# Kernel tuning notes

Measured on AMD Instinct MI355X. Metric: run time of the kernel, lower is better.

The kernel has to match this reference:

```python
import jax, jax.numpy as jnp
import numpy as np

N, D, S, C = 2048, 1024, 49, 1000


def setup_inputs() -> dict:
    key = jax.random.key(0)
    k1, k2, k3 = jax.random.split(key, 3)
    x = jax.random.normal(k1, (N, D, S), dtype=jnp.float32)
    mu = jax.random.normal(k2, (C, D), dtype=jnp.float32)
    # precision = inverse covariance -> symmetric PSD; build a well-conditioned one
    R = jax.random.normal(k3, (D, D), dtype=jnp.float32)
    precision = (R @ R.T) / D + jnp.eye(D, dtype=jnp.float32)
    return {"x": x, "mu": mu, "precision": precision}


def reference(x, mu, precision):
    # z: [N, D] global-average-pooled features (z.view(N, D, -1).mean(2))
    z = jnp.mean(x, axis=2)
    # score[n, c] = -0.5 * (z_n - mu_c) @ P @ (z_n - mu_c)
    # Expanded to avoid materializing [N, C, D]:
    #   zPz - z P mu - mu P z + mu P mu   (no symmetry assumption on P)
    zP = z @ precision                      # [N, D]
    zPt = z @ precision.T                   # [N, D]
    qz = jnp.sum(zP * z, axis=1)            # [N]   diag(z P z^T)
    cross1 = zP @ mu.T                      # [N, C] z P mu
    cross2 = zPt @ mu.T                     # [N, C] mu P z
    qmu = jnp.einsum('cd,de,ce->c', mu, precision, mu)  # [C]
    score = -0.5 * (qz[:, None] - cross1 - cross2 + qmu[None, :])
    return score
```

## Files before the change

### kernel.cpp

```cpp
#include <hip/hip_runtime.h>
#include <hip/hip_bf16.h>

typedef unsigned short u16;
typedef __bf16 bf16x8 __attribute__((ext_vector_type(8)));
typedef float f32x4 __attribute__((ext_vector_type(4)));

typedef const __attribute__((address_space(1))) void gv_t;
typedef __attribute__((address_space(3))) void lv_t;

#define NN 2048
#define DD 1024
#define SS 49
#define CC 1000
#define CP 1024

#define BK 64
#define KK DD

__device__ inline u16 f2bf(float f) {
    __hip_bfloat16 h = __float2bfloat16(f);
    union { __hip_bfloat16 h; u16 u; } cv; cv.h = h; return cv.u;
}

__device__ __forceinline__ void gemm64_core(const u16* __restrict__ A,
                                            const u16* __restrict__ Bt,
                                            int m0, int n0, char* smem,
                                            f32x4 acc[2][2], int tid) {
    char* As = smem;
    char* Bs = smem + 16384;
    const int lane = tid & 63;
    const int wr = (tid >> 6) >> 1, wc = (tid >> 6) & 1;
    const int r16 = lane & 15, hk = lane >> 4;
    const char* Ab = (const char*)A;
    const char* Bb = (const char*)Bt;

    auto stage = [&](int buf, int k0) {
        #pragma unroll
        for (int j = 0; j < 2; j++) {
            const int c = j * 256 + tid;
            const int row = c >> 3, slot = c & 7;
            const int goff = ((slot ^ (row & 7)) << 4);
            __builtin_amdgcn_global_load_lds(
                (gv_t*)(Ab + ((size_t)(m0 + row) * KK + k0) * 2 + goff),
                (lv_t*)(As + buf * 8192 + c * 16), 16, 0, 0);
            __builtin_amdgcn_global_load_lds(
                (gv_t*)(Bb + ((size_t)(n0 + row) * KK + k0) * 2 + goff),
                (lv_t*)(Bs + buf * 8192 + c * 16), 16, 0, 0);
        }
    };

    const int nt = KK / BK;
    stage(0, 0);
    __syncthreads();
    int cur = 0;
    for (int kt = 0; kt < nt; ++kt) {
        if (kt + 1 < nt) stage(cur ^ 1, (kt + 1) * BK);
        bf16x8 a[2][2], b[2][2];
        #pragma unroll
        for (int mi = 0; mi < 2; mi++) {
            const int row = wr * 32 + mi * 16 + r16;
            #pragma unroll
            for (int kk2 = 0; kk2 < 2; kk2++) {
                const int g = kk2 * 4 + hk;
                a[mi][kk2] = *(const bf16x8*)(As + cur * 8192 + row * 128 + ((g ^ (row & 7)) << 4));
            }
        }
        #pragma unroll
        for (int ni = 0; ni < 2; ni++) {
            const int row = wc * 32 + ni * 16 + r16;
            #pragma unroll
            for (int kk2 = 0; kk2 < 2; kk2++) {
                const int g = kk2 * 4 + hk;
                b[ni][kk2] = *(const bf16x8*)(Bs + cur * 8192 + row * 128 + ((g ^ (row & 7)) << 4));
            }
        }
        #pragma unroll
        for (int kk2 = 0; kk2 < 2; kk2++)
            #pragma unroll
            for (int mi = 0; mi < 2; mi++)
                #pragma unroll
                for (int ni = 0; ni < 2; ni++)
                    acc[mi][ni] = __builtin_amdgcn_mfma_f32_16x16x32_bf16(
                        a[mi][kk2], b[ni][kk2], acc[mi][ni], 0, 0, 0);
        __syncthreads();
        cur ^= 1;
    }
}

__global__ __launch_bounds__(256) void prep_k(const float* __restrict__ P,
                                              const float* __restrict__ mu,
                                              u16* __restrict__ q,
                                              u16* __restrict__ mu_bf,
                                              float* __restrict__ qzh,
                                              float* __restrict__ qmuh) {
    int i = blockIdx.x * 256 + threadIdx.x;
    int r = i >> 10, c = i & 1023;
    q[i]     = f2bf(P[i] + P[c * DD + r]);
    mu_bf[i] = f2bf(r < CC ? mu[i] : 0.f);
    if (i < NN) qzh[i]  = 0.f;
    if (i < CP) qmuh[i] = 0.f;
}

__global__ __launch_bounds__(256) void pool_muq_k(const float* __restrict__ x,
                                                  const u16* __restrict__ q,
                                                  const u16* __restrict__ mu_bf,
                                                  const float* __restrict__ mu,
                                                  u16* __restrict__ b_bf,
                                                  float* __restrict__ qmuh,
                                                  float* __restrict__ zf,
                                                  u16* __restrict__ zb) {
    __shared__ char smem[50176];
    const int tid = threadIdx.x;
    const int bid = blockIdx.x;

    if (bid >= 256) {
        const int u = bid - 256;
        float* lds = (float*)smem;
        const size_t base = (size_t)u * (256 * SS);
        const float4* src = (const float4*)(x + base);
        float4* dst = (float4*)lds;
        #pragma unroll
        for (int i = 0; i < 13; i++) {
            int idx = i * 256 + tid;
            if (idx < (256 * SS) / 4) dst[idx] = src[idx];
        }
        __syncthreads();
        const float* r = lds + tid * SS;
        float s = 0.f;
        #pragma unroll
        for (int j = 0; j < SS; j++) s += r[j];
        s *= (1.f / 49.f);
        size_t o = (size_t)u * 256 + tid;
        zf[o] = s;
        zb[o] = f2bf(s);
        return;
    }

    const int m0 = (bid >> 4) * 64, n0 = (bid & 15) * 64;
    f32x4 acc[2][2] = {};
    gemm64_core(mu_bf, q, m0, n0, smem, acc, tid);

    const int lane = tid & 63;
    const int wr = (tid >> 6) >> 1, wc = (tid >> 6) & 1;
    const int cr = (lane >> 4) * 4, cc2 = lane & 15;
    #pragma unroll
    for (int mi = 0; mi < 2; mi++) {
        const int gr0 = m0 + wr * 32 + mi * 16 + cr;
        #pragma unroll
        for (int r = 0; r < 4; r++) {
            const int row = gr0 + r;
            float v = 0.f;
            #pragma unroll
            for (int ni = 0; ni < 2; ni++) {
                const int gc = n0 + wc * 32 + ni * 16 + cc2;
                float av = acc[mi][ni][r];
                float sv = (row < CC) ? mu[(size_t)row * DD + gc] : 0.f;
                v += av * sv;
                b_bf[(size_t)row * DD + gc] = f2bf(av);
            }
            #pragma unroll
            for (int m = 1; m < 16; m <<= 1) v += __shfl_xor(v, m);
            if (cc2 == 0) atomicAdd(qmuh + row, 0.25f * v);
        }
    }
}

__global__ __launch_bounds__(256) void zgemm_k(const u16* __restrict__ z_bf,
                                               const u16* __restrict__ q,
                                               const u16* __restrict__ b_bf,
                                               const float* __restrict__ zf,
                                               const float* __restrict__ qmuh,
                                               float* __restrict__ qzh,
                                               float* __restrict__ part) {
    __shared__ char smem[32768];
    const int tid = threadIdx.x;
    const int bid = blockIdx.x;
    const bool isScore = (bid < 512);
    const int i = isScore ? bid : bid - 512;
    const int m0 = (i >> 4) * 64, n0 = (i & 15) * 64;

    f32x4 acc[2][2] = {};
    gemm64_core(z_bf, isScore ? b_bf : q, m0, n0, smem, acc, tid);

    const int lane = tid & 63;
    const int wr = (tid >> 6) >> 1, wc = (tid >> 6) & 1;
    const int cr = (lane >> 4) * 4, cc2 = lane & 15;
    if (isScore) {
        #pragma unroll
        for (int mi = 0; mi < 2; mi++) {
            #pragma unroll
            for (int ni = 0; ni < 2; ni++) {
                const int gr = m0 + wr * 32 + mi * 16 + cr;
                const int gc = n0 + wc * 32 + ni * 16 + cc2;
                const float qm = qmuh[gc];
                #pragma unroll
                for (int r = 0; r < 4; r++)
                    part[(size_t)(gr + r) * CP + gc] = 0.5f * acc[mi][ni][r] - qm;
            }
        }
    } else {
        #pragma unroll
        for (int mi = 0; mi < 2; mi++) {
            const int gr0 = m0 + wr * 32 + mi * 16 + cr;
            #pragma unroll
            for (int r = 0; r < 4; r++) {
                const int row = gr0 + r;
                float v = 0.f;
                #pragma unroll
                for (int ni = 0; ni < 2; ni++) {
                    const int gc = n0 + wc * 32 + ni * 16 + cc2;
                    v += acc[mi][ni][r] * zf[(size_t)row * DD + gc];
                }
                #pragma unroll
                for (int m = 1; m < 16; m <<= 1) v += __shfl_xor(v, m);
                if (cc2 == 0) atomicAdd(qzh + row, 0.25f * v);
            }
        }
    }
}

__global__ __launch_bounds__(256) void finish_k(const float* __restrict__ part,
                                                const float* __restrict__ qzh,
                                                float* __restrict__ out) {
    const int n = blockIdx.x, tid = threadIdx.x;
    if (tid >= 250) return;
    const float qz = qzh[n];
    float4 p = *(const float4*)(part + (size_t)n * CP + tid * 4);
    float4 o = { p.x - qz, p.y - qz, p.z - qz, p.w - qz };
    *(float4*)(out + (size_t)n * CC + tid * 4) = o;
}

extern "C" void kernel_launch(void* const* d_in, const int* in_sizes, int n_in,
                              void* d_out, int out_size, void* d_ws, size_t ws_size,
                              hipStream_t stream) {
    const float* x  = (const float*)d_in[0];
    const float* mu = (const float*)d_in[1];
    const float* P  = (const float*)d_in[2];
    float* out = (float*)d_out;

    char* w = (char*)d_ws;
    u16*   q_bf  = (u16*)w;   w += (size_t)DD * DD * 2;
    u16*   mu_bf = (u16*)w;   w += (size_t)CP * DD * 2;
    u16*   b_bf  = (u16*)w;   w += (size_t)CP * DD * 2;
    u16*   z_bf  = (u16*)w;   w += (size_t)NN * DD * 2;
    float* zf    = (float*)w; w += (size_t)NN * DD * 4;
    float* part  = (float*)w; w += (size_t)NN * CP * 4;
    float* qzh   = (float*)w; w += (size_t)NN * 4;
    float* qmuh  = (float*)w;

    prep_k<<<(DD * DD) / 256, 256, 0, stream>>>(P, mu, q_bf, mu_bf, qzh, qmuh);
    pool_muq_k<<<256 + (NN * DD) / 256, 256, 0, stream>>>(
        x, q_bf, mu_bf, mu, b_bf, qmuh, zf, z_bf);
    zgemm_k<<<1024, 256, 0, stream>>>(z_bf, q_bf, b_bf, zf, qmuh, qzh, part);
    finish_k<<<NN, 256, 0, stream>>>(part, qzh, out);
}
```

Baseline: 119.3 us.

## Restage kernels to overlap pooling with GEMMs and triple-buffer the GEMM core

Pooling of x is split across two launches. The first half runs alongside the precision/mu conversion, and the second half runs alongside the mu·Q GEMM and the first half of the z·Q GEMM. The score GEMM is split by row halves so that it writes the final output directly, with qz and qmu subtracted in its epilogue. This removes the partial buffer and the finish kernel. The GEMM inner loop moves from double to triple buffering, with explicit vmcnt waits and a single barrier per k-step, which raises shared memory use to 48KB per block.

```diff
diff --git a/kernel.cpp b/kernel.cpp
--- a/kernel.cpp
+++ b/kernel.cpp
@@ -16,6 +16,7 @@
 
 #define BK 64
 #define KK DD
+#define NT (KK / BK)
 
 __device__ inline u16 f2bf(float f) {
     __hip_bfloat16 h = __float2bfloat16(f);
@@ -26,8 +27,6 @@
                                             const u16* __restrict__ Bt,
                                             int m0, int n0, char* smem,
                                             f32x4 acc[2][2], int tid) {
-    char* As = smem;
-    char* Bs = smem + 16384;
     const int lane = tid & 63;
     const int wr = (tid >> 6) >> 1, wc = (tid >> 6) & 1;
     const int r16 = lane & 15, hk = lane >> 4;
@@ -42,19 +41,24 @@
             const int goff = ((slot ^ (row & 7)) << 4);
             __builtin_amdgcn_global_load_lds(
                 (gv_t*)(Ab + ((size_t)(m0 + row) * KK + k0) * 2 + goff),
-                (lv_t*)(As + buf * 8192 + c * 16), 16, 0, 0);
+                (lv_t*)(smem + buf * 16384 + c * 16), 16, 0, 0);
             __builtin_amdgcn_global_load_lds(
                 (gv_t*)(Bb + ((size_t)(n0 + row) * KK + k0) * 2 + goff),
-                (lv_t*)(Bs + buf * 8192 + c * 16), 16, 0, 0);
+                (lv_t*)(smem + buf * 16384 + 8192 + c * 16), 16, 0, 0);
         }
     };
 
-    const int nt = KK / BK;
     stage(0, 0);
-    __syncthreads();
-    int cur = 0;
-    for (int kt = 0; kt < nt; ++kt) {
-        if (kt + 1 < nt) stage(cur ^ 1, (kt + 1) * BK);
+    stage(1, BK);
+    for (int t = 0; t < NT; ++t) {
+        if (t + 1 < NT) asm volatile("s_waitcnt vmcnt(4)" ::: "memory");
+        else            asm volatile("s_waitcnt vmcnt(0)" ::: "memory");
+        __builtin_amdgcn_s_barrier();
+        __builtin_amdgcn_sched_barrier(0);
+        if (t + 2 < NT) stage((t + 2) % 3, (t + 2) * BK);
+
+        const char* As = smem + (t % 3) * 16384;
+        const char* Bs = As + 8192;
         bf16x8 a[2][2], b[2][2];
         #pragma unroll
         for (int mi = 0; mi < 2; mi++) {
@@ -62,7 +66,7 @@
             #pragma unroll
             for (int kk2 = 0; kk2 < 2; kk2++) {
                 const int g = kk2 * 4 + hk;
-                a[mi][kk2] = *(const bf16x8*)(As + cur * 8192 + row * 128 + ((g ^ (row & 7)) << 4));
+                a[mi][kk2] = *(const bf16x8*)(As + row * 128 + ((g ^ (row & 7)) << 4));
             }
         }
         #pragma unroll
@@ -71,7 +75,7 @@
             #pragma unroll
             for (int kk2 = 0; kk2 < 2; kk2++) {
                 const int g = kk2 * 4 + hk;
-                b[ni][kk2] = *(const bf16x8*)(Bs + cur * 8192 + row * 128 + ((g ^ (row & 7)) << 4));
+                b[ni][kk2] = *(const bf16x8*)(Bs + row * 128 + ((g ^ (row & 7)) << 4));
             }
         }
         #pragma unroll
@@ -82,64 +86,37 @@
                 for (int ni = 0; ni < 2; ni++)
                     acc[mi][ni] = __builtin_amdgcn_mfma_f32_16x16x32_bf16(
                         a[mi][kk2], b[ni][kk2], acc[mi][ni], 0, 0, 0);
-        __syncthreads();
-        cur ^= 1;
-    }
-}
-
-__global__ __launch_bounds__(256) void prep_k(const float* __restrict__ P,
-                                              const float* __restrict__ mu,
-                                              u16* __restrict__ q,
-                                              u16* __restrict__ mu_bf,
-                                              float* __restrict__ qzh,
-                                              float* __restrict__ qmuh) {
-    int i = blockIdx.x * 256 + threadIdx.x;
-    int r = i >> 10, c = i & 1023;
-    q[i]     = f2bf(P[i] + P[c * DD + r]);
-    mu_bf[i] = f2bf(r < CC ? mu[i] : 0.f);
-    if (i < NN) qzh[i]  = 0.f;
-    if (i < CP) qmuh[i] = 0.f;
-}
-
-__global__ __launch_bounds__(256) void pool_muq_k(const float* __restrict__ x,
-                                                  const u16* __restrict__ q,
-                                                  const u16* __restrict__ mu_bf,
-                                                  const float* __restrict__ mu,
-                                                  u16* __restrict__ b_bf,
-                                                  float* __restrict__ qmuh,
-                                                  float* __restrict__ zf,
-                                                  u16* __restrict__ zb) {
-    __shared__ char smem[50176];
-    const int tid = threadIdx.x;
-    const int bid = blockIdx.x;
-
-    if (bid >= 256) {
-        const int u = bid - 256;
-        float* lds = (float*)smem;
-        const size_t base = (size_t)u * (256 * SS);
-        const float4* src = (const float4*)(x + base);
-        float4* dst = (float4*)lds;
-        #pragma unroll
-        for (int i = 0; i < 13; i++) {
-            int idx = i * 256 + tid;
-            if (idx < (256 * SS) / 4) dst[idx] = src[idx];
-        }
-        __syncthreads();
-        const float* r = lds + tid * SS;
-        float s = 0.f;
-        #pragma unroll
-        for (int j = 0; j < SS; j++) s += r[j];
-        s *= (1.f / 49.f);
-        size_t o = (size_t)u * 256 + tid;
-        zf[o] = s;
-        zb[o] = f2bf(s);
-        return;
-    }
-
-    const int m0 = (bid >> 4) * 64, n0 = (bid & 15) * 64;
-    f32x4 acc[2][2] = {};
-    gemm64_core(mu_bf, q, m0, n0, smem, acc, tid);
-
+    }
+}
+
+
+__device__ __forceinline__ void pool_unit(const float* __restrict__ x, int u,
+                                          float* __restrict__ zf,
+                                          u16* __restrict__ zb,
+                                          char* smem, int tid) {
+    float* lds = (float*)smem;
+    const size_t base = (size_t)u * (256 * SS);
+    const float4* src = (const float4*)(x + base);
+    float4* dst = (float4*)lds;
+    #pragma unroll
+    for (int i = 0; i < 13; i++) {
+        int idx = i * 256 + tid;
+        if (idx < (256 * SS) / 4) dst[idx] = src[idx];
+    }
+    __syncthreads();
+    const float* r = lds + tid * SS;
+    float s = 0.f;
+    #pragma unroll
+    for (int j = 0; j < SS; j++) s += r[j];
+    s *= (1.f / 49.f);
+    size_t o = (size_t)u * 256 + tid;
+    zf[o] = s;
+    zb[o] = f2bf(s);
+}
+
+__device__ __forceinline__ void zqd_epi(const f32x4 acc[2][2], int m0, int n0,
+                                        const float* __restrict__ zf,
+                                        float* __restrict__ qzh, int tid) {
     const int lane = tid & 63;
     const int wr = (tid >> 6) >> 1, wc = (tid >> 6) & 1;
     const int cr = (lane >> 4) * 4, cc2 = lane & 15;
@@ -153,52 +130,82 @@
             #pragma unroll
             for (int ni = 0; ni < 2; ni++) {
                 const int gc = n0 + wc * 32 + ni * 16 + cc2;
-                float av = acc[mi][ni][r];
-                float sv = (row < CC) ? mu[(size_t)row * DD + gc] : 0.f;
-                v += av * sv;
-                b_bf[(size_t)row * DD + gc] = f2bf(av);
+                v += acc[mi][ni][r] * zf[(size_t)row * DD + gc];
             }
             #pragma unroll
             for (int m = 1; m < 16; m <<= 1) v += __shfl_xor(v, m);
-            if (cc2 == 0) atomicAdd(qmuh + row, 0.25f * v);
-        }
-    }
-}
-
-__global__ __launch_bounds__(256) void zgemm_k(const u16* __restrict__ z_bf,
-                                               const u16* __restrict__ q,
-                                               const u16* __restrict__ b_bf,
-                                               const float* __restrict__ zf,
-                                               const float* __restrict__ qmuh,
-                                               float* __restrict__ qzh,
-                                               float* __restrict__ part) {
-    __shared__ char smem[32768];
-    const int tid = threadIdx.x;
-    const int bid = blockIdx.x;
-    const bool isScore = (bid < 512);
-    const int i = isScore ? bid : bid - 512;
-    const int m0 = (i >> 4) * 64, n0 = (i & 15) * 64;
-
-    f32x4 acc[2][2] = {};
-    gemm64_core(z_bf, isScore ? b_bf : q, m0, n0, smem, acc, tid);
-
+            if (cc2 == 0) atomicAdd(qzh + row, 0.25f * v);
+        }
+    }
+}
+
+__device__ __forceinline__ void score_epi(const f32x4 acc[2][2], int m0, int n0,
+                                          const float* __restrict__ qzh,
+                                          const float* __restrict__ qmuh,
+                                          float* __restrict__ out, int tid) {
     const int lane = tid & 63;
     const int wr = (tid >> 6) >> 1, wc = (tid >> 6) & 1;
     const int cr = (lane >> 4) * 4, cc2 = lane & 15;
-    if (isScore) {
-        #pragma unroll
-        for (int mi = 0; mi < 2; mi++) {
-            #pragma unroll
-            for (int ni = 0; ni < 2; ni++) {
-                const int gr = m0 + wr * 32 + mi * 16 + cr;
-                const int gc = n0 + wc * 32 + ni * 16 + cc2;
+    #pragma unroll
+    for (int mi = 0; mi < 2; mi++) {
+        #pragma unroll
+        for (int ni = 0; ni < 2; ni++) {
+            const int gr = m0 + wr * 32 + mi * 16 + cr;
+            const int gc = n0 + wc * 32 + ni * 16 + cc2;
+            if (gc < CC) {
                 const float qm = qmuh[gc];
                 #pragma unroll
                 for (int r = 0; r < 4; r++)
-                    part[(size_t)(gr + r) * CP + gc] = 0.5f * acc[mi][ni][r] - qm;
-            }
-        }
+                    out[(size_t)(gr + r) * CC + gc] =
+                        0.5f * acc[mi][ni][r] - qzh[gr + r] - qm;
+            }
+        }
+    }
+}
+
+__global__ __launch_bounds__(256) void l1a_k(const float* __restrict__ x,
+                                             const float* __restrict__ P,
+                                             const float* __restrict__ mu,
+                                             u16* __restrict__ q,
+                                             u16* __restrict__ mu_bf,
+                                             float* __restrict__ zf,
+                                             u16* __restrict__ zb,
+                                             float* __restrict__ qzh,
+                                             float* __restrict__ qmuh) {
+    __shared__ char smem[50176];
+    const int tid = threadIdx.x, bid = blockIdx.x;
+    if (bid < 4096) {
+        int i = bid * 256 + tid;
+        int r = i >> 10, c = i & 1023;
+        q[i]     = f2bf(P[i] + P[c * DD + r]);
+        mu_bf[i] = f2bf(r < CC ? mu[i] : 0.f);
+        if (i < NN) qzh[i]  = 0.f;
+        if (i < CP) qmuh[i] = 0.f;
     } else {
+        pool_unit(x, bid - 4096, zf, zb, smem, tid);
+    }
+}
+
+__global__ __launch_bounds__(256) void l1b_k(const float* __restrict__ x,
+                                             const u16* __restrict__ q,
+                                             const u16* __restrict__ mu_bf,
+                                             const float* __restrict__ mu,
+                                             const u16* __restrict__ z_bf,
+                                             u16* __restrict__ b_bf,
+                                             float* __restrict__ qmuh,
+                                             const float* __restrict__ zf,
+                                             float* __restrict__ zf_w,
+                                             u16* __restrict__ zb_w,
+                                             float* __restrict__ qzh) {
+    __shared__ char smem[50176];
+    const int tid = threadIdx.x, bid = blockIdx.x;
+    if (bid < 256) {
+        const int m0 = (bid >> 4) * 64, n0 = (bid & 15) * 64;
+        f32x4 acc[2][2] = {};
+        gemm64_core(mu_bf, q, m0, n0, smem, acc, tid);
+        const int lane = tid & 63;
+        const int wr = (tid >> 6) >> 1, wc = (tid >> 6) & 1;
+        const int cr = (lane >> 4) * 4, cc2 = lane & 15;
         #pragma unroll
         for (int mi = 0; mi < 2; mi++) {
             const int gr0 = m0 + wr * 32 + mi * 16 + cr;
@@ -209,25 +216,61 @@
                 #pragma unroll
                 for (int ni = 0; ni < 2; ni++) {
                     const int gc = n0 + wc * 32 + ni * 16 + cc2;
-                    v += acc[mi][ni][r] * zf[(size_t)row * DD + gc];
+                    float av = acc[mi][ni][r];
+                    float sv = (row < CC) ? mu[(size_t)row * DD + gc] : 0.f;
+                    v += av * sv;
+                    b_bf[(size_t)row * DD + gc] = f2bf(av);
                 }
                 #pragma unroll
                 for (int m = 1; m < 16; m <<= 1) v += __shfl_xor(v, m);
-                if (cc2 == 0) atomicAdd(qzh + row, 0.25f * v);
-            }
-        }
-    }
-}
-
-__global__ __launch_bounds__(256) void finish_k(const float* __restrict__ part,
-                                                const float* __restrict__ qzh,
-                                                float* __restrict__ out) {
-    const int n = blockIdx.x, tid = threadIdx.x;
-    if (tid >= 250) return;
-    const float qz = qzh[n];
-    float4 p = *(const float4*)(part + (size_t)n * CP + tid * 4);
-    float4 o = { p.x - qz, p.y - qz, p.z - qz, p.w - qz };
-    *(float4*)(out + (size_t)n * CC + tid * 4) = o;
+                if (cc2 == 0) atomicAdd(qmuh + row, 0.25f * v);
+            }
+        }
+    } else if (bid < 512) {
+        const int i = bid - 256;
+        const int m0 = (i >> 4) * 64, n0 = (i & 15) * 64;
+        f32x4 acc[2][2] = {};
+        gemm64_core(z_bf, q, m0, n0, smem, acc, tid);
+        zqd_epi(acc, m0, n0, zf, qzh, tid);
+    } else {
+        pool_unit(x, bid - 512 + 4096, zf_w, zb_w, smem, tid);
+    }
+}
+
+__global__ __launch_bounds__(256) void l2_k(const u16* __restrict__ z_bf,
+                                            const u16* __restrict__ q,
+                                            const u16* __restrict__ b_bf,
+                                            const float* __restrict__ zf,
+                                            float* __restrict__ qzh,
+                                            const float* __restrict__ qmuh,
+                                            float* __restrict__ out) {
+    __shared__ char smem[49152];
+    const int tid = threadIdx.x, bid = blockIdx.x;
+    if (bid < 256) {
+        const int m0 = 1024 + (bid >> 4) * 64, n0 = (bid & 15) * 64;
+        f32x4 acc[2][2] = {};
+        gemm64_core(z_bf, q, m0, n0, smem, acc, tid);
+        zqd_epi(acc, m0, n0, zf, qzh, tid);
+    } else {
+        const int i = bid - 256;
+        const int m0 = (i >> 4) * 64, n0 = (i & 15) * 64;
+        f32x4 acc[2][2] = {};
+        gemm64_core(z_bf, b_bf, m0, n0, smem, acc, tid);
+        score_epi(acc, m0, n0, qzh, qmuh, out, tid);
+    }
+}
+
+__global__ __launch_bounds__(256) void l3_k(const u16* __restrict__ z_bf,
+                                            const u16* __restrict__ b_bf,
+                                            const float* __restrict__ qzh,
+                                            const float* __restrict__ qmuh,
+                                            float* __restrict__ out) {
+    __shared__ char smem[49152];
+    const int tid = threadIdx.x, bid = blockIdx.x;
+    const int m0 = 1024 + (bid >> 4) * 64, n0 = (bid & 15) * 64;
+    f32x4 acc[2][2] = {};
+    gemm64_core(z_bf, b_bf, m0, n0, smem, acc, tid);
+    score_epi(acc, m0, n0, qzh, qmuh, out, tid);
 }
 
 extern "C" void kernel_launch(void* const* d_in, const int* in_sizes, int n_in,
@@ -244,13 +287,12 @@
     u16*   b_bf  = (u16*)w;   w += (size_t)CP * DD * 2;
     u16*   z_bf  = (u16*)w;   w += (size_t)NN * DD * 2;
     float* zf    = (float*)w; w += (size_t)NN * DD * 4;
-    float* part  = (float*)w; w += (size_t)NN * CP * 4;
     float* qzh   = (float*)w; w += (size_t)NN * 4;
     float* qmuh  = (float*)w;
 
-    prep_k<<<(DD * DD) / 256, 256, 0, stream>>>(P, mu, q_bf, mu_bf, qzh, qmuh);
-    pool_muq_k<<<256 + (NN * DD) / 256, 256, 0, stream>>>(
-        x, q_bf, mu_bf, mu, b_bf, qmuh, zf, z_bf);
-    zgemm_k<<<1024, 256, 0, stream>>>(z_bf, q_bf, b_bf, zf, qmuh, qzh, part);
-    finish_k<<<NN, 256, 0, stream>>>(part, qzh, out);
-}
+    l1a_k<<<8192, 256, 0, stream>>>(x, P, mu, q_bf, mu_bf, zf, z_bf, qzh, qmuh);
+    l1b_k<<<4608, 256, 0, stream>>>(x, q_bf, mu_bf, mu, z_bf, b_bf, qmuh,
+                                    zf, zf, z_bf, qzh);
+    l2_k<<<512, 256, 0, stream>>>(z_bf, q_bf, b_bf, zf, qzh, qmuh, out);
+    l3_k<<<256, 256, 0, stream>>>(z_bf, b_bf, qzh, qmuh, out);
+}
```

Result: slower. 122.3 us (+2.6%).

## Triple-buffer GEMM K-loop, persistent pooling with async LDS loads, write scores directly

Applied to the files above, without the earlier changes.

The shared 64x64 GEMM core moves from a double-buffered loop with two barriers per step to a three-stage ring, using explicit vmcnt waits and one barrier per K-step, so global-to-LDS loads stay two tiles ahead. The pooling branch becomes a persistent loop over 768 blocks that double-buffers half-tiles of x through direct global-to-LDS loads, aiming to overlap HBM reads of the 400MB input with the reductions. The score GEMM now writes into the output with the qmu term applied, and a fixup kernel subtracts qz in place, which drops the padded intermediate buffer. The trade-offs are more LDS per block (48KB), which may lower occupancy, and only half the threads doing pooling arithmetic.

```diff
diff --git a/kernel.cpp b/kernel.cpp
--- a/kernel.cpp
+++ b/kernel.cpp
@@ -16,6 +16,12 @@
 
 #define BK 64
 #define KK DD
+#define NT (KK / BK)
+
+#define HALF_BYTES  25088
+#define HALF_CHUNKS 1568
+#define N_HALVES    ((NN * DD) / 128)
+#define POOL_BLKS   768
 
 __device__ inline u16 f2bf(float f) {
     __hip_bfloat16 h = __float2bfloat16(f);
@@ -26,8 +32,6 @@
                                             const u16* __restrict__ Bt,
                                             int m0, int n0, char* smem,
                                             f32x4 acc[2][2], int tid) {
-    char* As = smem;
-    char* Bs = smem + 16384;
     const int lane = tid & 63;
     const int wr = (tid >> 6) >> 1, wc = (tid >> 6) & 1;
     const int r16 = lane & 15, hk = lane >> 4;
@@ -42,19 +46,24 @@
             const int goff = ((slot ^ (row & 7)) << 4);
             __builtin_amdgcn_global_load_lds(
                 (gv_t*)(Ab + ((size_t)(m0 + row) * KK + k0) * 2 + goff),
-                (lv_t*)(As + buf * 8192 + c * 16), 16, 0, 0);
+                (lv_t*)(smem + buf * 16384 + c * 16), 16, 0, 0);
             __builtin_amdgcn_global_load_lds(
                 (gv_t*)(Bb + ((size_t)(n0 + row) * KK + k0) * 2 + goff),
-                (lv_t*)(Bs + buf * 8192 + c * 16), 16, 0, 0);
+                (lv_t*)(smem + buf * 16384 + 8192 + c * 16), 16, 0, 0);
         }
     };
 
-    const int nt = KK / BK;
     stage(0, 0);
-    __syncthreads();
-    int cur = 0;
-    for (int kt = 0; kt < nt; ++kt) {
-        if (kt + 1 < nt) stage(cur ^ 1, (kt + 1) * BK);
+    stage(1, BK);
+    for (int t = 0; t < NT; ++t) {
+        if (t + 1 < NT) asm volatile("s_waitcnt vmcnt(4)" ::: "memory");
+        else            asm volatile("s_waitcnt vmcnt(0)" ::: "memory");
+        __builtin_amdgcn_s_barrier();
+        __builtin_amdgcn_sched_barrier(0);
+        if (t + 2 < NT) stage((t + 2) % 3, (t + 2) * BK);
+
+        const char* As = smem + (t % 3) * 16384;
+        const char* Bs = As + 8192;
         bf16x8 a[2][2], b[2][2];
         #pragma unroll
         for (int mi = 0; mi < 2; mi++) {
@@ -62,7 +71,7 @@
             #pragma unroll
             for (int kk2 = 0; kk2 < 2; kk2++) {
                 const int g = kk2 * 4 + hk;
-                a[mi][kk2] = *(const bf16x8*)(As + cur * 8192 + row * 128 + ((g ^ (row & 7)) << 4));
+                a[mi][kk2] = *(const bf16x8*)(As + row * 128 + ((g ^ (row & 7)) << 4));
             }
         }
         #pragma unroll
@@ -71,7 +80,7 @@
             #pragma unroll
             for (int kk2 = 0; kk2 < 2; kk2++) {
                 const int g = kk2 * 4 + hk;
-                b[ni][kk2] = *(const bf16x8*)(Bs + cur * 8192 + row * 128 + ((g ^ (row & 7)) << 4));
+                b[ni][kk2] = *(const bf16x8*)(Bs + row * 128 + ((g ^ (row & 7)) << 4));
             }
         }
         #pragma unroll
@@ -82,8 +91,6 @@
                 for (int ni = 0; ni < 2; ni++)
                     acc[mi][ni] = __builtin_amdgcn_mfma_f32_16x16x32_bf16(
                         a[mi][kk2], b[ni][kk2], acc[mi][ni], 0, 0, 0);
-        __syncthreads();
-        cur ^= 1;
     }
 }
 
@@ -114,25 +121,45 @@
     const int bid = blockIdx.x;
 
     if (bid >= 256) {
-        const int u = bid - 256;
-        float* lds = (float*)smem;
-        const size_t base = (size_t)u * (256 * SS);
-        const float4* src = (const float4*)(x + base);
-        float4* dst = (float4*)lds;
-        #pragma unroll
-        for (int i = 0; i < 13; i++) {
-            int idx = i * 256 + tid;
-            if (idx < (256 * SS) / 4) dst[idx] = src[idx];
-        }
-        __syncthreads();
-        const float* r = lds + tid * SS;
-        float s = 0.f;
-        #pragma unroll
-        for (int j = 0; j < SS; j++) s += r[j];
-        s *= (1.f / 49.f);
-        size_t o = (size_t)u * 256 + tid;
-        zf[o] = s;
-        zb[o] = f2bf(s);
+        const int pb = bid - 256;
+        char* bufA = smem;
+        char* bufB = smem + HALF_BYTES;
+        const char* xb = (const char*)x;
+
+        auto issue = [&](char* buf, int H) {
+            const char* src = xb + (size_t)H * HALF_BYTES;
+            #pragma unroll
+            for (int i = 0; i < 7; i++) {
+                const int c = i * 256 + tid;
+                if (c < HALF_CHUNKS)
+                    __builtin_amdgcn_global_load_lds(
+                        (gv_t*)(src + c * 16), (lv_t*)(buf + c * 16), 16, 0, 0);
+            }
+        };
+
+        int H = pb;
+        char* cur = bufA;
+        char* nxt = bufB;
+        issue(cur, H);
+        while (H < N_HALVES) {
+            asm volatile("s_waitcnt vmcnt(0)" ::: "memory");
+            __builtin_amdgcn_s_barrier();
+            __builtin_amdgcn_sched_barrier(0);
+            const int Hn = H + POOL_BLKS;
+            if (Hn < N_HALVES) issue(nxt, Hn);
+            if (tid < 128) {
+                const float* row = (const float*)cur + tid * SS;
+                float s = 0.f;
+                #pragma unroll
+                for (int j = 0; j < SS; j++) s += row[j];
+                s *= (1.f / 49.f);
+                const size_t o = (size_t)H * 128 + tid;
+                zf[o] = s;
+                zb[o] = f2bf(s);
+            }
+            char* t_ = cur; cur = nxt; nxt = t_;
+            H = Hn;
+        }
         return;
     }
 
@@ -169,36 +196,20 @@
                                                const u16* __restrict__ q,
                                                const u16* __restrict__ b_bf,
                                                const float* __restrict__ zf,
+                                               float* __restrict__ qzh,
                                                const float* __restrict__ qmuh,
-                                               float* __restrict__ qzh,
-                                               float* __restrict__ part) {
-    __shared__ char smem[32768];
+                                               float* __restrict__ out) {
+    __shared__ char smem[49152];
     const int tid = threadIdx.x;
     const int bid = blockIdx.x;
-    const bool isScore = (bid < 512);
-    const int i = isScore ? bid : bid - 512;
-    const int m0 = (i >> 4) * 64, n0 = (i & 15) * 64;
-
-    f32x4 acc[2][2] = {};
-    gemm64_core(z_bf, isScore ? b_bf : q, m0, n0, smem, acc, tid);
-
     const int lane = tid & 63;
     const int wr = (tid >> 6) >> 1, wc = (tid >> 6) & 1;
     const int cr = (lane >> 4) * 4, cc2 = lane & 15;
-    if (isScore) {
-        #pragma unroll
-        for (int mi = 0; mi < 2; mi++) {
-            #pragma unroll
-            for (int ni = 0; ni < 2; ni++) {
-                const int gr = m0 + wr * 32 + mi * 16 + cr;
-                const int gc = n0 + wc * 32 + ni * 16 + cc2;
-                const float qm = qmuh[gc];
-                #pragma unroll
-                for (int r = 0; r < 4; r++)
-                    part[(size_t)(gr + r) * CP + gc] = 0.5f * acc[mi][ni][r] - qm;
-            }
-        }
-    } else {
+
+    if (bid < 512) {
+        const int m0 = (bid >> 4) * 64, n0 = (bid & 15) * 64;
+        f32x4 acc[2][2] = {};
+        gemm64_core(z_bf, q, m0, n0, smem, acc, tid);
         #pragma unroll
         for (int mi = 0; mi < 2; mi++) {
             const int gr0 = m0 + wr * 32 + mi * 16 + cr;
@@ -216,18 +227,38 @@
                 if (cc2 == 0) atomicAdd(qzh + row, 0.25f * v);
             }
         }
-    }
-}
-
-__global__ __launch_bounds__(256) void finish_k(const float* __restrict__ part,
-                                                const float* __restrict__ qzh,
-                                                float* __restrict__ out) {
+    } else {
+        const int i = bid - 512;
+        const int m0 = (i >> 4) * 64, n0 = (i & 15) * 64;
+        f32x4 acc[2][2] = {};
+        gemm64_core(z_bf, b_bf, m0, n0, smem, acc, tid);
+        #pragma unroll
+        for (int mi = 0; mi < 2; mi++) {
+            #pragma unroll
+            for (int ni = 0; ni < 2; ni++) {
+                const int gr = m0 + wr * 32 + mi * 16 + cr;
+                const int gc = n0 + wc * 32 + ni * 16 + cc2;
+                if (gc < CC) {
+                    const float qm = qmuh[gc];
+                    #pragma unroll
+                    for (int r = 0; r < 4; r++)
+                        out[(size_t)(gr + r) * CC + gc] =
+                            0.5f * acc[mi][ni][r] - qm;
+                }
+            }
+        }
+    }
+}
+
+__global__ __launch_bounds__(256) void fixup_k(float* __restrict__ out,
+                                               const float* __restrict__ qzh) {
     const int n = blockIdx.x, tid = threadIdx.x;
     if (tid >= 250) return;
     const float qz = qzh[n];
-    float4 p = *(const float4*)(part + (size_t)n * CP + tid * 4);
-    float4 o = { p.x - qz, p.y - qz, p.z - qz, p.w - qz };
-    *(float4*)(out + (size_t)n * CC + tid * 4) = o;
+    float4* p = (float4*)(out + (size_t)n * CC + tid * 4);
+    float4 v = *p;
+    v.x -= qz; v.y -= qz; v.z -= qz; v.w -= qz;
+    *p = v;
 }
 
 extern "C" void kernel_launch(void* const* d_in, const int* in_sizes, int n_in,
@@ -244,13 +275,12 @@
     u16*   b_bf  = (u16*)w;   w += (size_t)CP * DD * 2;
     u16*   z_bf  = (u16*)w;   w += (size_t)NN * DD * 2;
     float* zf    = (float*)w; w += (size_t)NN * DD * 4;
-    float* part  = (float*)w; w += (size_t)NN * CP * 4;
     float* qzh   = (float*)w; w += (size_t)NN * 4;
     float* qmuh  = (float*)w;
 
     prep_k<<<(DD * DD) / 256, 256, 0, stream>>>(P, mu, q_bf, mu_bf, qzh, qmuh);
-    pool_muq_k<<<256 + (NN * DD) / 256, 256, 0, stream>>>(
+    pool_muq_k<<<256 + POOL_BLKS, 256, 0, stream>>>(
         x, q_bf, mu_bf, mu, b_bf, qmuh, zf, z_bf);
-    zgemm_k<<<1024, 256, 0, stream>>>(z_bf, q_bf, b_bf, zf, qmuh, qzh, part);
-    finish_k<<<NN, 256, 0, stream>>>(part, qzh, out);
-}
+    zgemm_k<<<1024, 256, 0, stream>>>(z_bf, q_bf, b_bf, zf, qzh, qmuh, out);
+    fixup_k<<<NN, 256, 0, stream>>>(out, qzh);
+}
```

Result: no change. 120.1 us (+0.7%).
